# Optimization experiments

Measured on AMD Instinct MI355X. Metric: run time of the kernel, lower is better.

Reference implementation:

```python
import jax, jax.numpy as jnp
import numpy as np

B = 512          # batch == number of memories
S = 8            # num_attention_splits
U = 512          # num_units = sum(num_units_regions)
D = 32           # dim_attention_unit
G = 8            # num_attention_groups
MASK_P = 0.1
DIM_IN = 4096
DAG = 2048       # dim_attention_global


def setup_inputs() -> dict:
    key = jax.random.key(0)
    ks = jax.random.split(key, 8)
    # xavier-normal-ish scales for the unit-wise linears
    s1 = (2.0 / (DIM_IN // S + DAG // S)) ** 0.5
    s2 = (2.0 / (DAG // S + U * D // S)) ** 0.5
    return {
        "x": jax.random.normal(ks[0], (B, DIM_IN), jnp.float32),
        "mem_attention": jax.random.normal(ks[1], (B, U, D), jnp.float32),
        "mem_outputs": jax.random.normal(ks[2], (B, U, D), jnp.float32),
        "rand_u": jax.random.uniform(ks[3], (B, B, U), jnp.float32),
        "w1": jax.random.normal(ks[4], (S, DIM_IN // S, DAG // S), jnp.float32) * s1,
        "b1": jnp.zeros((S, DAG // S), jnp.float32),
        "w2": jax.random.normal(ks[5], (S, DAG // S, U * D // S), jnp.float32) * s2,
        "b2": jnp.zeros((S, U * D // S), jnp.float32),
        "temperature": jnp.ones((U,), jnp.float32),
    }


def reference(x, mem_attention, mem_outputs, rand_u, w1, b1, w2, b2, temperature):
    # attentions(): split input, two unit-wise linears
    xs = x.reshape(B, S, DIM_IN // S)                        # [B,S,I/S]
    ga = jnp.einsum("bsi,sio->bso", xs, w1) + b1             # [B,S,DAG/S]
    att = jnp.einsum("bso,soj->bsj", ga, w2) + b2            # [B,S,U*D/S]
    att = att.reshape(B, U, D)                               # [B,U,D]
    ga_flat = ga.reshape(B, DAG)                             # [B,DAG]

    # per-unit pairwise scores: (att_b . mem_att_m) per unit  -> [B,M,U]
    weights = jnp.einsum("bud,mud->bmu", att, mem_attention)
    weights = weights * temperature                          # broadcast over U

    neg_inf = jnp.float32(-jnp.inf)
    weights = jnp.where(rand_u < MASK_P, neg_inf, weights)   # random mask
    eye = jnp.eye(B, dtype=bool)[:, :, None]                 # self-exclusion
    weights = jnp.where(eye, neg_inf, weights)

    # group-wise softmax over the memory axis
    w = weights.reshape(B, B // G, G, U)
    w = jax.nn.softmax(w, axis=1)
    w = w.reshape(B, B, U) / 8.0

    # weighted reduction over memories (avoids [B,B,U,D] intermediate)
    outputs = jnp.einsum("bmu,mud->bud", w, mem_outputs)     # [B,U,D]
    return att, ga_flat, w, outputs
```

## Files before the change

### kernel.cpp

```cpp
#include <hip/hip_runtime.h>
#include <math.h>

#define NEGBIG (-1e30f)


__global__ __launch_bounds__(256) void gemm_split(
    const float* __restrict__ A, int lda, int Ksz,
    const float* __restrict__ Bw, int NS,
    const float* __restrict__ bias,
    float* __restrict__ C, int ldc)
{
  const int n0 = blockIdx.x * 64;
  const int b0 = blockIdx.y * 64;
  const int s  = n0 / NS;
  const float* Bp = Bw + (size_t)s * Ksz * NS;
  const int nloc0 = n0 - s * NS;
  const int acol0 = s * Ksz;

  __shared__ float As[16][64];
  __shared__ float Bs[16][64];

  const int t  = threadIdx.x;
  const int tb = t & 15, tn = t >> 4;
  float acc[4][4] = {};

  for (int k0 = 0; k0 < Ksz; k0 += 16) {
    {
      int r = t & 63, g = t >> 6;
      float4 v = *reinterpret_cast<const float4*>(
          A + (size_t)(b0 + r) * lda + acol0 + k0 + 4 * g);
      As[4*g+0][r] = v.x; As[4*g+1][r] = v.y; As[4*g+2][r] = v.z; As[4*g+3][r] = v.w;
    }
    {
      int kk = t >> 4, n4 = t & 15;
      float4 v = *reinterpret_cast<const float4*>(
          Bp + (size_t)(k0 + kk) * NS + nloc0 + 4 * n4);
      *reinterpret_cast<float4*>(&Bs[kk][4*n4]) = v;
    }
    __syncthreads();
#pragma unroll
    for (int k = 0; k < 16; ++k) {
      float4 a4 = *reinterpret_cast<const float4*>(&As[k][4*tb]);
      float4 b4 = *reinterpret_cast<const float4*>(&Bs[k][4*tn]);
      float av[4] = {a4.x, a4.y, a4.z, a4.w};
      float bv[4] = {b4.x, b4.y, b4.z, b4.w};
#pragma unroll
      for (int i = 0; i < 4; ++i)
#pragma unroll
        for (int j = 0; j < 4; ++j)
          acc[i][j] = fmaf(av[i], bv[j], acc[i][j]);
    }
    __syncthreads();
  }
#pragma unroll
  for (int i = 0; i < 4; ++i) {
    int row = b0 + 4*tb + i;
    int col = n0 + 4*tn;
    float4 o;
    o.x = acc[i][0] + bias[col + 0];
    o.y = acc[i][1] + bias[col + 1];
    o.z = acc[i][2] + bias[col + 2];
    o.w = acc[i][3] + bias[col + 3];
    *reinterpret_cast<float4*>(C + (size_t)row * ldc + col) = o;
  }
}

__global__ __launch_bounds__(256) void scores_stats_kernel(
    const float* __restrict__ att,
    const float* __restrict__ ma,
    const float* __restrict__ rnd,
    const float* __restrict__ temp,
    float* __restrict__ wout,
    float* __restrict__ stats)
{
  __shared__ float At[16 * 516];
  __shared__ float Ma[16 * 260];
  const int b0 = blockIdx.x * 16;
  const int u0 = blockIdx.y * 16;
  const int t  = threadIdx.x;
  const int u  = t & 15, tb = (t >> 4) & 3, tm = t >> 6;

  {
    int r = t >> 4, base = t & 15;
    const float* src = att + (size_t)(b0 + r) * 16384 + u0 * 32;
#pragma unroll
    for (int g = 0; g < 8; ++g) {
      int i4 = base + 16 * g;
      int uu = i4 >> 3, d4 = i4 & 7;
      float4 v = *reinterpret_cast<const float4*>(src + 4 * i4);
      *reinterpret_cast<float4*>(&At[uu*516 + d4*64 + (r ^ ((2*d4) & 15))*4]) = v;
    }
  }
  const float tmp = temp[u0 + u];
  float Ms[4][2], Ls[4][2];
#pragma unroll
  for (int i = 0; i < 4; ++i)
#pragma unroll
    for (int j = 0; j < 2; ++j) { Ms[i][j] = NEGBIG; Ls[i][j] = 0.f; }

  for (int m0 = 0; m0 < 512; m0 += 8) {
    float rv[4][2];
#pragma unroll
    for (int i = 0; i < 4; ++i)
#pragma unroll
      for (int j = 0; j < 2; ++j)
        rv[i][j] = rnd[((size_t)(b0 + 4*tb + i) * 512 + m0 + 2*tm + j) * 512 + u0 + u];
    __syncthreads();
    {
      int r = t >> 5, base = t & 31;
      const float* src = ma + (size_t)(m0 + r) * 16384 + u0 * 32;
#pragma unroll
      for (int g = 0; g < 4; ++g) {
        int i4 = base + 32 * g;
        int uu = i4 >> 3, d4 = i4 & 7;
        float4 v = *reinterpret_cast<const float4*>(src + 4 * i4);
        *reinterpret_cast<float4*>(&Ma[uu*260 + d4*32 + ((r ^ d4) & 7)*4]) = v;
      }
    }
    __syncthreads();
    float acc[4][2] = {};
#pragma unroll
    for (int d4 = 0; d4 < 8; ++d4) {
      const int sw = (2*d4) & 15;
      float4 av[4], mv[2];
#pragma unroll
      for (int i = 0; i < 4; ++i)
        av[i] = *reinterpret_cast<const float4*>(&At[u*516 + d4*64 + ((4*tb+i) ^ sw)*4]);
#pragma unroll
      for (int j = 0; j < 2; ++j)
        mv[j] = *reinterpret_cast<const float4*>(&Ma[u*260 + d4*32 + (((2*tm+j) ^ d4) & 7)*4]);
#pragma unroll
      for (int i = 0; i < 4; ++i)
#pragma unroll
        for (int j = 0; j < 2; ++j) {
          acc[i][j] = fmaf(av[i].x, mv[j].x, acc[i][j]);
          acc[i][j] = fmaf(av[i].y, mv[j].y, acc[i][j]);
          acc[i][j] = fmaf(av[i].z, mv[j].z, acc[i][j]);
          acc[i][j] = fmaf(av[i].w, mv[j].w, acc[i][j]);
        }
    }
#pragma unroll
    for (int i = 0; i < 4; ++i)
#pragma unroll
      for (int j = 0; j < 2; ++j) {
        int gb = b0 + 4*tb + i, gm = m0 + 2*tm + j;
        float s = acc[i][j] * tmp;
        if ((rv[i][j] < 0.1f) | (gm == gb)) s = NEGBIG;
        wout[((size_t)gb * 512 + gm) * 512 + u0 + u] = s;
        float d = s - Ms[i][j];
        if (d > 0.f) { Ls[i][j] = fmaf(Ls[i][j], __expf(-d), 1.f); Ms[i][j] = s; }
        else          Ls[i][j] += __expf(d);
      }
  }
#pragma unroll
  for (int i = 0; i < 4; ++i)
#pragma unroll
    for (int j = 0; j < 2; ++j) {
      int b = b0 + 4*tb + i, g = 2*tm + j;
      float* cell = stats + ((size_t)b * 512 + u0 + u) * 32;
      cell[g]     = Ms[i][j];
      cell[8 + g] = 1.0f / (8.0f * Ls[i][j]);
    }
}

__global__ __launch_bounds__(256) void emit_outputs_v2(
    const float* __restrict__ mo,
    float* __restrict__ w,
    float* __restrict__ outs)
{
  __shared__ float MoL[8 * 16 * 32];
  __shared__ float E[8 * 16 * 17];
  const int u0 = blockIdx.x * 16;
  const int b0 = blockIdx.y * 16;
  const int t  = threadIdx.x;
  const int ab = t >> 4, am = (t >> 1) & 7, uh = t & 1;
  const int pu = t >> 4, bq = (t >> 2) & 3, dh = t & 3;

  float Mreg[8], Sreg[8];
  {
    const float* cb = outs + ((size_t)(b0 + ab) * 512 + u0 + uh * 8) * 32;
#pragma unroll
    for (int j = 0; j < 8; ++j) {
      Mreg[j] = cb[j * 32 + am];
      Sreg[j] = cb[j * 32 + 8 + am];
    }
  }

  float4 acc[4][2];
#pragma unroll
  for (int i = 0; i < 4; ++i) {
    acc[i][0] = make_float4(0.f, 0.f, 0.f, 0.f);
    acc[i][1] = make_float4(0.f, 0.f, 0.f, 0.f);
  }

  float* wbase = w + (size_t)(b0 + ab) * 262144 + u0 + uh * 8;

  const float* msrc0;  const float* msrc1;  const float* msrc2;  const float* msrc3;
  int loff0, loff1, loff2, loff3;
  {
    int P, mm, uu, dq;
    P = t;          mm = P >> 7; uu = (P >> 3) & 15; dq = P & 7;
    msrc0 = mo + (size_t)mm * 16384 + (size_t)(u0 + uu) * 32 + (dq ^ (uu & 7)) * 4;
    loff0 = P * 4;
    P = 256 + t;    mm = P >> 7; uu = (P >> 3) & 15; dq = P & 7;
    msrc1 = mo + (size_t)mm * 16384 + (size_t)(u0 + uu) * 32 + (dq ^ (uu & 7)) * 4;
    loff1 = P * 4;
    P = 512 + t;    mm = P >> 7; uu = (P >> 3) & 15; dq = P & 7;
    msrc2 = mo + (size_t)mm * 16384 + (size_t)(u0 + uu) * 32 + (dq ^ (uu & 7)) * 4;
    loff2 = P * 4;
    P = 768 + t;    mm = P >> 7; uu = (P >> 3) & 15; dq = P & 7;
    msrc3 = mo + (size_t)mm * 16384 + (size_t)(u0 + uu) * 32 + (dq ^ (uu & 7)) * 4;
    loff3 = P * 4;
  }

  float4 wpre0, wpre1, smo0, smo1, smo2, smo3;
  {
    const float* wp = wbase + (size_t)am * 512;
    wpre0 = *reinterpret_cast<const float4*>(wp);
    wpre1 = *reinterpret_cast<const float4*>(wp + 4);
    smo0 = *reinterpret_cast<const float4*>(msrc0);
    smo1 = *reinterpret_cast<const float4*>(msrc1);
    smo2 = *reinterpret_cast<const float4*>(msrc2);
    smo3 = *reinterpret_cast<const float4*>(msrc3);
  }

#pragma unroll 1
  for (int c = 0; c < 64; ++c) {
    const int mc = c * 8;
    if (c) __syncthreads();

    {
      float* wp = wbase + (size_t)(mc + am) * 512;
      float s0[4] = {wpre0.x, wpre0.y, wpre0.z, wpre0.w};
      float s1[4] = {wpre1.x, wpre1.y, wpre1.z, wpre1.w};
#pragma unroll
      for (int e2 = 0; e2 < 4; ++e2) {
        float v = __expf(s0[e2] - Mreg[e2]) * Sreg[e2];
        s0[e2] = v;
        E[(am * 16 + uh * 8 + e2) * 17 + ab] = v;
      }
#pragma unroll
      for (int e2 = 0; e2 < 4; ++e2) {
        float v = __expf(s1[e2] - Mreg[4 + e2]) * Sreg[4 + e2];
        s1[e2] = v;
        E[(am * 16 + uh * 8 + 4 + e2) * 17 + ab] = v;
      }
      *reinterpret_cast<float4*>(wp)     = make_float4(s0[0], s0[1], s0[2], s0[3]);
      *reinterpret_cast<float4*>(wp + 4) = make_float4(s1[0], s1[1], s1[2], s1[3]);
    }
    *reinterpret_cast<float4*>(&MoL[loff0]) = smo0;
    *reinterpret_cast<float4*>(&MoL[loff1]) = smo1;
    *reinterpret_cast<float4*>(&MoL[loff2]) = smo2;
    *reinterpret_cast<float4*>(&MoL[loff3]) = smo3;
    __syncthreads();

    if (c < 63) {
      const float* wp = wbase + (size_t)(mc + 8 + am) * 512;
      wpre0 = *reinterpret_cast<const float4*>(wp);
      wpre1 = *reinterpret_cast<const float4*>(wp + 4);
      const size_t moff = (size_t)(mc + 8) * 16384;
      smo0 = *reinterpret_cast<const float4*>(msrc0 + moff);
      smo1 = *reinterpret_cast<const float4*>(msrc1 + moff);
      smo2 = *reinterpret_cast<const float4*>(msrc2 + moff);
      smo3 = *reinterpret_cast<const float4*>(msrc3 + moff);
    }

#pragma unroll
    for (int m = 0; m < 8; ++m) {
      float4 ef = *reinterpret_cast<const float4*>(&E[(m * 16 + pu) * 17 + 4 * bq]);
      float4 v0 = *reinterpret_cast<const float4*>(
          &MoL[(m * 16 + pu) * 32 + (((2 * dh) ^ (pu & 7)) * 4)]);
      float4 v1 = *reinterpret_cast<const float4*>(
          &MoL[(m * 16 + pu) * 32 + (((2 * dh + 1) ^ (pu & 7)) * 4)]);
      float es[4] = {ef.x, ef.y, ef.z, ef.w};
#pragma unroll
      for (int i = 0; i < 4; ++i) {
        acc[i][0].x = fmaf(es[i], v0.x, acc[i][0].x);
        acc[i][0].y = fmaf(es[i], v0.y, acc[i][0].y);
        acc[i][0].z = fmaf(es[i], v0.z, acc[i][0].z);
        acc[i][0].w = fmaf(es[i], v0.w, acc[i][0].w);
        acc[i][1].x = fmaf(es[i], v1.x, acc[i][1].x);
        acc[i][1].y = fmaf(es[i], v1.y, acc[i][1].y);
        acc[i][1].z = fmaf(es[i], v1.z, acc[i][1].z);
        acc[i][1].w = fmaf(es[i], v1.w, acc[i][1].w);
      }
    }
  }

#pragma unroll
  for (int i = 0; i < 4; ++i) {
    float* dst = outs + ((size_t)(b0 + 4 * bq + i) * 512 + u0 + pu) * 32 + 8 * dh;
    *reinterpret_cast<float4*>(dst)     = acc[i][0];
    *reinterpret_cast<float4*>(dst + 4) = acc[i][1];
  }
}

extern "C" void kernel_launch(void* const* d_in, const int* in_sizes, int n_in,
                              void* d_out, int out_size, void* d_ws, size_t ws_size,
                              hipStream_t stream) {
  const float* x    = (const float*)d_in[0];
  const float* ma   = (const float*)d_in[1];
  const float* mo   = (const float*)d_in[2];
  const float* rnd  = (const float*)d_in[3];
  const float* w1   = (const float*)d_in[4];
  const float* b1   = (const float*)d_in[5];
  const float* w2   = (const float*)d_in[6];
  const float* b2   = (const float*)d_in[7];
  const float* temp = (const float*)d_in[8];

  float* out  = (float*)d_out;
  float* att  = out;
  float* ga   = out + 8388608;
  float* wbuf = out + 9437184;
  float* outs = out + 143654912;

  gemm_split<<<dim3(32, 8), 256, 0, stream>>>(x, 4096, 512, w1, 256, b1, ga, 2048);
  gemm_split<<<dim3(256, 8), 256, 0, stream>>>(ga, 2048, 256, w2, 2048, b2, att, 16384);
  scores_stats_kernel<<<dim3(32, 32), 256, 0, stream>>>(att, ma, rnd, temp, wbuf, outs);
  emit_outputs_v2<<<dim3(32, 32), 256, 0, stream>>>(mo, wbuf, outs);
}
```

Measured before the change: 830.9 us.

## Compute pairwise unit scores with split-bf16 MFMA and coalesced row-wise writes

Replaces the FP32 FMA score kernel with one that computes per-unit attention dot products through bf16 MFMA instructions. It uses a hi/lo split (three MFMAs) to keep close to FP32 accuracy. Results are transposed through shared memory so each thread owns one (b,m) row and writes 16 contiguous units as float4, with the next random-mask tile prefetched. Softmax max/sum statistics are merged across lanes with shuffles at the end. The aim is to cut ALU cost and improve global write coalescing, at the price of a small precision loss and extra conversion work per tile.

```diff
diff --git a/kernel.cpp b/kernel.cpp
--- a/kernel.cpp
+++ b/kernel.cpp
@@ -2,6 +2,9 @@
 #include <math.h>
 
 #define NEGBIG (-1e30f)
+
+typedef __bf16 bf16x8 __attribute__((ext_vector_type(8)));
+typedef float  f32x4  __attribute__((ext_vector_type(4)));
 
 
 __global__ __launch_bounds__(256) void gemm_split(
@@ -65,7 +68,7 @@
   }
 }
 
-__global__ __launch_bounds__(256) void scores_stats_kernel(
+__global__ __launch_bounds__(256) void scores_stats_mfma(
     const float* __restrict__ att,
     const float* __restrict__ ma,
     const float* __restrict__ rnd,
@@ -73,94 +76,126 @@
     float* __restrict__ wout,
     float* __restrict__ stats)
 {
-  __shared__ float At[16 * 516];
-  __shared__ float Ma[16 * 260];
+  __shared__ float tr[256 * 17];
   const int b0 = blockIdx.x * 16;
   const int u0 = blockIdx.y * 16;
   const int t  = threadIdx.x;
-  const int u  = t & 15, tb = (t >> 4) & 3, tm = t >> 6;
-
-  {
-    int r = t >> 4, base = t & 15;
-    const float* src = att + (size_t)(b0 + r) * 16384 + u0 * 32;
-#pragma unroll
-    for (int g = 0; g < 8; ++g) {
-      int i4 = base + 16 * g;
-      int uu = i4 >> 3, d4 = i4 & 7;
-      float4 v = *reinterpret_cast<const float4*>(src + 4 * i4);
-      *reinterpret_cast<float4*>(&At[uu*516 + d4*64 + (r ^ ((2*d4) & 15))*4]) = v;
-    }
-  }
-  const float tmp = temp[u0 + u];
-  float Ms[4][2], Ls[4][2];
-#pragma unroll
-  for (int i = 0; i < 4; ++i)
-#pragma unroll
-    for (int j = 0; j < 2; ++j) { Ms[i][j] = NEGBIG; Ls[i][j] = 0.f; }
-
-  for (int m0 = 0; m0 < 512; m0 += 8) {
-    float rv[4][2];
-#pragma unroll
-    for (int i = 0; i < 4; ++i)
-#pragma unroll
-      for (int j = 0; j < 2; ++j)
-        rv[i][j] = rnd[((size_t)(b0 + 4*tb + i) * 512 + m0 + 2*tm + j) * 512 + u0 + u];
-    __syncthreads();
+  const int w  = t >> 6, l = t & 63;
+  const int lo16 = l & 15, kb = l >> 4;
+  const int bl = t >> 4, ml = t & 15;
+  const int gb = b0 + bl;
+
+  float tvf[16];
+#pragma unroll
+  for (int q = 0; q < 4; ++q) {
+    float4 tq = *reinterpret_cast<const float4*>(temp + u0 + 4 * q);
+    tvf[4*q+0] = tq.x; tvf[4*q+1] = tq.y; tvf[4*q+2] = tq.z; tvf[4*q+3] = tq.w;
+  }
+
+  bf16x8 Ahi[4], Alo[4];
+#pragma unroll
+  for (int q = 0; q < 4; ++q) {
+    const float* ap = att + (size_t)(b0 + lo16) * 16384
+                    + (size_t)(u0 + 4 * w + q) * 32 + kb * 8;
+    float4 a0 = *reinterpret_cast<const float4*>(ap);
+    float4 a1 = *reinterpret_cast<const float4*>(ap + 4);
+    float af[8] = {a0.x, a0.y, a0.z, a0.w, a1.x, a1.y, a1.z, a1.w};
+#pragma unroll
+    for (int j = 0; j < 8; ++j) {
+      __bf16 h = (__bf16)af[j];
+      Ahi[q][j] = h;
+      Alo[q][j] = (__bf16)(af[j] - (float)h);
+    }
+  }
+
+  float M[16], L[16];
+#pragma unroll
+  for (int u = 0; u < 16; ++u) { M[u] = NEGBIG; L[u] = 0.f; }
+
+  const float* rb = rnd  + (size_t)gb * 262144 + u0;
+  float*       wb = wout + (size_t)gb * 262144 + u0;
+
+  float4 rv[4], rnx[4];
+#pragma unroll
+  for (int q = 0; q < 4; ++q)
+    rv[q] = *reinterpret_cast<const float4*>(rb + (size_t)ml * 512 + 4 * q);
+
+#pragma unroll 1
+  for (int c = 0; c < 32; ++c) {
+    const int m0 = c * 16;
+
+#pragma unroll
+    for (int q = 0; q < 4; ++q) {
+      const float* bp = ma + (size_t)(m0 + lo16) * 16384
+                      + (size_t)(u0 + 4 * w + q) * 32 + kb * 8;
+      float4 b0v = *reinterpret_cast<const float4*>(bp);
+      float4 b1v = *reinterpret_cast<const float4*>(bp + 4);
+      float bf[8] = {b0v.x, b0v.y, b0v.z, b0v.w, b1v.x, b1v.y, b1v.z, b1v.w};
+      bf16x8 Bhi, Blo;
+#pragma unroll
+      for (int j = 0; j < 8; ++j) {
+        __bf16 h = (__bf16)bf[j];
+        Bhi[j] = h;
+        Blo[j] = (__bf16)(bf[j] - (float)h);
+      }
+      f32x4 acc = {0.f, 0.f, 0.f, 0.f};
+      acc = __builtin_amdgcn_mfma_f32_16x16x32_bf16(Ahi[q], Blo, acc, 0, 0, 0);
+      acc = __builtin_amdgcn_mfma_f32_16x16x32_bf16(Alo[q], Bhi, acc, 0, 0, 0);
+      acc = __builtin_amdgcn_mfma_f32_16x16x32_bf16(Ahi[q], Bhi, acc, 0, 0, 0);
+#pragma unroll
+      for (int i = 0; i < 4; ++i)
+        tr[((kb * 4 + i) * 16 + lo16) * 17 + 4 * w + q] = acc[i];
+    }
+    __syncthreads();
+
+    if (c < 31) {
+#pragma unroll
+      for (int q = 0; q < 4; ++q)
+        rnx[q] = *reinterpret_cast<const float4*>(
+            rb + (size_t)(m0 + 16 + ml) * 512 + 4 * q);
+    }
+
+    const int gm = m0 + ml;
+    const bool dg = (gm == gb);
+    float sv[16];
+#pragma unroll
+    for (int q = 0; q < 4; ++q) {
+      float rr[4] = {rv[q].x, rv[q].y, rv[q].z, rv[q].w};
+#pragma unroll
+      for (int e = 0; e < 4; ++e) {
+        const int u = 4 * q + e;
+        float s = tr[t * 17 + u] * tvf[u];
+        if ((rr[e] < 0.1f) | dg) s = NEGBIG;
+        sv[u] = s;
+        float d = s - M[u];
+        if (d > 0.f) { L[u] = fmaf(L[u], __expf(-d), 1.f); M[u] = s; }
+        else          L[u] += __expf(d);
+      }
+    }
     {
-      int r = t >> 5, base = t & 31;
-      const float* src = ma + (size_t)(m0 + r) * 16384 + u0 * 32;
-#pragma unroll
-      for (int g = 0; g < 4; ++g) {
-        int i4 = base + 32 * g;
-        int uu = i4 >> 3, d4 = i4 & 7;
-        float4 v = *reinterpret_cast<const float4*>(src + 4 * i4);
-        *reinterpret_cast<float4*>(&Ma[uu*260 + d4*32 + ((r ^ d4) & 7)*4]) = v;
-      }
-    }
-    __syncthreads();
-    float acc[4][2] = {};
-#pragma unroll
-    for (int d4 = 0; d4 < 8; ++d4) {
-      const int sw = (2*d4) & 15;
-      float4 av[4], mv[2];
-#pragma unroll
-      for (int i = 0; i < 4; ++i)
-        av[i] = *reinterpret_cast<const float4*>(&At[u*516 + d4*64 + ((4*tb+i) ^ sw)*4]);
-#pragma unroll
-      for (int j = 0; j < 2; ++j)
-        mv[j] = *reinterpret_cast<const float4*>(&Ma[u*260 + d4*32 + (((2*tm+j) ^ d4) & 7)*4]);
-#pragma unroll
-      for (int i = 0; i < 4; ++i)
-#pragma unroll
-        for (int j = 0; j < 2; ++j) {
-          acc[i][j] = fmaf(av[i].x, mv[j].x, acc[i][j]);
-          acc[i][j] = fmaf(av[i].y, mv[j].y, acc[i][j]);
-          acc[i][j] = fmaf(av[i].z, mv[j].z, acc[i][j]);
-          acc[i][j] = fmaf(av[i].w, mv[j].w, acc[i][j]);
-        }
-    }
-#pragma unroll
-    for (int i = 0; i < 4; ++i)
-#pragma unroll
-      for (int j = 0; j < 2; ++j) {
-        int gb = b0 + 4*tb + i, gm = m0 + 2*tm + j;
-        float s = acc[i][j] * tmp;
-        if ((rv[i][j] < 0.1f) | (gm == gb)) s = NEGBIG;
-        wout[((size_t)gb * 512 + gm) * 512 + u0 + u] = s;
-        float d = s - Ms[i][j];
-        if (d > 0.f) { Ls[i][j] = fmaf(Ls[i][j], __expf(-d), 1.f); Ms[i][j] = s; }
-        else          Ls[i][j] += __expf(d);
-      }
-  }
-#pragma unroll
-  for (int i = 0; i < 4; ++i)
-#pragma unroll
-    for (int j = 0; j < 2; ++j) {
-      int b = b0 + 4*tb + i, g = 2*tm + j;
-      float* cell = stats + ((size_t)b * 512 + u0 + u) * 32;
-      cell[g]     = Ms[i][j];
-      cell[8 + g] = 1.0f / (8.0f * Ls[i][j]);
-    }
+      float* wp = wb + (size_t)gm * 512;
+#pragma unroll
+      for (int q = 0; q < 4; ++q)
+        *reinterpret_cast<float4*>(wp + 4 * q) =
+            make_float4(sv[4*q], sv[4*q+1], sv[4*q+2], sv[4*q+3]);
+    }
+    __syncthreads();
+#pragma unroll
+    for (int q = 0; q < 4; ++q) rv[q] = rnx[q];
+  }
+
+#pragma unroll
+  for (int u = 0; u < 16; ++u) {
+    float oM = __shfl_xor(M[u], 8, 64);
+    float oL = __shfl_xor(L[u], 8, 64);
+    float nm = fmaxf(M[u], oM);
+    float Lm = L[u] * __expf(M[u] - nm) + oL * __expf(oM - nm);
+    if ((t & 8) == 0) {
+      float* cell = stats + ((size_t)gb * 512 + u0 + u) * 32;
+      cell[t & 7]       = nm;
+      cell[8 + (t & 7)] = 1.0f / (8.0f * Lm);
+    }
+  }
 }
 
 __global__ __launch_bounds__(256) void emit_outputs_v2(
@@ -316,6 +351,6 @@
 
   gemm_split<<<dim3(32, 8), 256, 0, stream>>>(x, 4096, 512, w1, 256, b1, ga, 2048);
   gemm_split<<<dim3(256, 8), 256, 0, stream>>>(ga, 2048, 256, w2, 2048, b2, att, 16384);
-  scores_stats_kernel<<<dim3(32, 32), 256, 0, stream>>>(att, ma, rnd, temp, wbuf, outs);
+  scores_stats_mfma<<<dim3(32, 32), 256, 0, stream>>>(att, ma, rnd, temp, wbuf, outs);
   emit_outputs_v2<<<dim3(32, 32), 256, 0, stream>>>(mo, wbuf, outs);
 }
```

Measured after the change: 922.2 us. +11.0%, slower.
